# Optimization experiments

Hardware: AMD Instinct MI355X
Metric: run time of the kernel (lower is better)

## Reference

```python
import jax, jax.numpy as jnp
import numpy as np

N = 8000      # num_nodes
U = 64        # num_units
D = 2         # input_dim
K = 2         # max_diffusion_step
E = 64000     # edges per support
B = 32        # batch
F = D + U     # concat feature size = 66
M = 2 * K + 1 # num_matrices = 5


def setup_inputs() -> dict:
    key = jax.random.key(0)
    ks = jax.random.split(key, 10)
    return {
        "inputs": jax.random.normal(ks[0], (B, N * D), dtype=jnp.float32),
        "hx": jax.random.normal(ks[1], (B, N * U), dtype=jnp.float32),
        "row0": jax.random.randint(ks[2], (E,), 0, N, dtype=jnp.int32),
        "col0": jax.random.randint(ks[3], (E,), 0, N, dtype=jnp.int32),
        "val0": jax.random.uniform(ks[4], (E,), dtype=jnp.float32) / 8.0,
        "row1": jax.random.randint(ks[5], (E,), 0, N, dtype=jnp.int32),
        "col1": jax.random.randint(ks[6], (E,), 0, N, dtype=jnp.int32),
        "val1": jax.random.uniform(ks[7], (E,), dtype=jnp.float32) / 8.0,
        "W_ru": jax.random.normal(ks[8], (F * M, 2 * U), dtype=jnp.float32) * 0.05,
        "b_ru": jnp.ones((2 * U,), dtype=jnp.float32),  # bias_start=1.0
        "W_c": jax.random.normal(ks[9], (F * M, U), dtype=jnp.float32) * 0.05,
        "b_c": jnp.zeros((U,), dtype=jnp.float32),       # bias_start=0.0
    }


def _spmm(row, col, val, x):
    # y[r] += val_e * x[c]  for each edge e=(r,c); x: [N, F*B]
    return jax.ops.segment_sum(val[:, None] * x[col], row, num_segments=N)


def _gconv(inputs, state, W, b, supports, output_size):
    # inputs: [B, N*D_in], state: [B, N*D_st]
    x = jnp.concatenate([inputs.reshape(B, N, -1), state.reshape(B, N, -1)], axis=2)  # [B,N,F]
    f = x.shape[2]
    x0 = x.transpose(1, 2, 0).reshape(N, f * B)  # [N, F*B]
    xs = [x0]
    for (row, col, val) in supports:
        x1 = _spmm(row, col, val, x0)
        xs.append(x1)
        xk_1, xk_2 = x1, x0
        for _ in range(2, K + 1):
            x2 = 2.0 * _spmm(row, col, val, xk_1) - xk_2
            xs.append(x2)
            xk_1, xk_2 = x2, xk_1
    m = len(xs)
    # [M,N,F,B] -> [B,N,F,M] -> [B*N, F*M]
    xc = jnp.stack(xs).reshape(m, N, f, B).transpose(3, 1, 2, 0).reshape(B * N, f * m)
    out = xc @ W + b
    return out.reshape(B, N * output_size)


def reference(inputs, hx, row0, col0, val0, row1, col1, val1, W_ru, b_ru, W_c, b_c):
    supports = ((row0, col0, val0), (row1, col1, val1))
    # reset/update gates via graph convolution
    value = jax.nn.sigmoid(_gconv(inputs, hx, W_ru, b_ru, supports, 2 * U))
    value = value.reshape(B, N, 2 * U)
    r = value[..., :U].reshape(B, N * U)
    u = value[..., U:].reshape(B, N * U)
    c = jnp.tanh(_gconv(inputs, r * hx, W_c, b_c, supports, U))
    new_state = u * hx + (1.0 - u) * c
    return new_state
```

## Files before the change

kernel.cpp:

```cpp
#include <hip/hip_runtime.h>
#include <stdint.h>

#define NN 8000
#define UU 64
#define EE 64000
#define BB 32
#define NB 256000
#define HXS 512000
#define SLAB4 256000
#define NT 8

typedef __attribute__((ext_vector_type(8))) __bf16 bf16x8;
typedef __attribute__((ext_vector_type(4))) float f32x4;

__device__ __forceinline__ unsigned short f2bf(float f){
  unsigned int u = __builtin_bit_cast(unsigned int, f);
  u += 0x7fffu + ((u >> 16) & 1u);
  return (unsigned short)(u >> 16);
}
__device__ __forceinline__ unsigned int pack2(float a, float b){
  return (unsigned int)f2bf(a) | ((unsigned int)f2bf(b) << 16);
}
__device__ __forceinline__ float bflo(unsigned int w){ return __builtin_bit_cast(float, w << 16); }
__device__ __forceinline__ float bfhi(unsigned int w){ return __builtin_bit_cast(float, w & 0xffff0000u); }
__device__ __forceinline__ float bfu(unsigned short v){ return __builtin_bit_cast(float, (unsigned int)v << 16); }

__device__ __forceinline__ void acc8(float* a, float v, uint4 q){
  a[0]+=v*bflo(q.x); a[1]+=v*bfhi(q.x); a[2]+=v*bflo(q.y); a[3]+=v*bfhi(q.y);
  a[4]+=v*bflo(q.z); a[5]+=v*bfhi(q.z); a[6]+=v*bflo(q.w); a[7]+=v*bfhi(q.w);
}

__device__ __forceinline__ void stage16(const unsigned short* g, unsigned short* ldsbase){
  __builtin_amdgcn_global_load_lds((const __attribute__((address_space(1))) void*)g,
                                   (__attribute__((address_space(3))) void*)ldsbase, 16, 0, 0);
}

__global__ void k_hist(const int* __restrict__ r0, const int* __restrict__ r1, int* __restrict__ cnt){
  int i = blockIdx.x * 256 + threadIdx.x;
  if (i < 2*EE){
    int s = (i >= EE);
    int r = s ? r1[i - EE] : r0[i];
    atomicAdd(&cnt[s*NN + r], 1);
  }
}

__global__ __launch_bounds__(1024) void k_scan(const int* __restrict__ cnt, int* __restrict__ row_ptr, int* __restrict__ rp_work){
  int sup = blockIdx.x;
  const int* c = cnt + sup*NN;
  __shared__ int part[1024];
  int t = threadIdx.x;
  int loc[8]; int s = 0;
  #pragma unroll
  for (int j=0;j<8;j++){ int idx=t*8+j; int v = (idx<NN)? c[idx]:0; loc[j]=s; s+=v; }
  part[t]=s; __syncthreads();
  for (int o=1;o<1024;o<<=1){
    int v = (t>=o)? part[t-o]:0;
    __syncthreads();
    part[t]+=v;
    __syncthreads();
  }
  int pre = (t>0)? part[t-1]:0;
  #pragma unroll
  for (int j=0;j<8;j++){ int idx=t*8+j; if(idx<NN){ int e=pre+loc[j]; row_ptr[sup*(NN+1)+idx]=e; rp_work[sup*NN+idx]=e; } }
  if (t==1023) row_ptr[sup*(NN+1)+NN] = part[1023];
}

__global__ void k_scatter(const int* __restrict__ r0, const int* __restrict__ c0, const float* __restrict__ v0,
                          const int* __restrict__ r1, const int* __restrict__ c1, const float* __restrict__ v1,
                          int* __restrict__ rp_work, int* __restrict__ col_s, float* __restrict__ val_s){
  int i = blockIdx.x * 256 + threadIdx.x;
  if (i < 2*EE){
    int s = (i >= EE);
    int e = s ? i - EE : i;
    int r  = s ? r1[e] : r0[e];
    int cc = s ? c1[e] : c0[e];
    float vv = s ? v1[e] : v0[e];
    int pos = atomicAdd(&rp_work[s*NN + r], 1);
    col_s[s*EE + pos] = cc;
    val_s[s*EE + pos] = vv;
  }
}

__global__ void k_wpack(const float* __restrict__ W_ru, const float* __restrict__ W_c,
                        unsigned short* __restrict__ Wru_t, unsigned short* __restrict__ Wc_t){
  int i = blockIdx.x * 256 + threadIdx.x;
  int k = i / 192; int oo = i % 192;
  const float* W; int ld, NC; unsigned short* dst; int c;
  if (oo < 128){ W = W_ru; ld = 128; NC = 128; dst = Wru_t; c = oo; }
  else         { W = W_c;  ld = 64;  NC = 64;  dst = Wc_t;  c = oo - 128; }
  int o = 4*(c & 15) + ((c >> 4) & 3);
  int wcol = (c >= 64) ? 64 + o : o;
  float v = 0.f;
  if (k < 330){
    int m, fb;
    if (k < 320){ m = k >> 6; fb = (2 + (k & 63)) * 5; }
    else        { int j = k - 320; m = j >> 1; fb = (j & 1) * 5; }
    if      (m==0) v = W[(fb+0)*ld+wcol] - W[(fb+2)*ld+wcol] - W[(fb+4)*ld+wcol];
    else if (m==1) v = W[(fb+1)*ld+wcol];
    else if (m==2) v = 2.f*W[(fb+2)*ld+wcol];
    else if (m==3) v = W[(fb+3)*ld+wcol];
    else           v = 2.f*W[(fb+4)*ld+wcol];
  }
  int dstoff;
  if (k < 320) dstoff = (k>>6)*NC*64 + c*64 + (k&63);
  else         dstoff = 320*NC + c*32 + (k-320);
  dst[dstoff] = f2bf(v);
}

__global__ void k_x0(const float* __restrict__ inputs, const float* __restrict__ hx,
                     uint4* __restrict__ xs0q, unsigned int* __restrict__ xi0){
  int n = blockIdx.x, t = threadIdx.x;
  int b = t >> 3, ug = t & 7;
  const float4 h0 = *(const float4*)(hx + (size_t)b*HXS + n*64 + ug*8);
  const float4 h1 = *(const float4*)(hx + (size_t)b*HXS + n*64 + ug*8 + 4);
  uint4 o;
  o.x = pack2(h0.x, h0.y); o.y = pack2(h0.z, h0.w);
  o.z = pack2(h1.x, h1.y); o.w = pack2(h1.z, h1.w);
  xs0q[(((size_t)(b>>2)*NN + n)*4 + (b&3))*8 + ug] = o;
  if (t < 32){
    int bb = t;
    const float2 g = *(const float2*)(inputs + (size_t)bb*(NN*2) + n*2);
    xi0[(((size_t)(bb>>2)*NN) + n)*4 + (bb&3)] = pack2(g.x, g.y);
  }
}

template<bool WITH_IN>
__global__ void k_spmm(const int* __restrict__ row_ptr, const int* __restrict__ col_s, const float* __restrict__ val_s,
                       uint4* xs4, uint4* xi4,
                       int srcA, int dstA, int srcB, int dstB){
  int bid = blockIdx.x;
  if (WITH_IN && bid >= 16000){
    int b2 = bid - 16000;
    int s = b2 & 7, supi = (b2 >> 3) & 1, chunk = b2 >> 4;
    int n = chunk*256 + threadIdx.x;
    if (n >= NN) return;
    int msrc = supi ? srcB : srcA, mdst = supi ? dstB : dstA;
    size_t sb = (size_t)(msrc*8 + s)*NN, db = (size_t)(mdst*8 + s)*NN;
    int beg = row_ptr[supi*(NN+1)+n], end = row_ptr[supi*(NN+1)+n+1];
    const int* cs = col_s + supi*EE; const float* vs = val_s + supi*EE;
    float ai[8] = {0.f,0.f,0.f,0.f,0.f,0.f,0.f,0.f};
    for (int e = beg; e < end; ++e){
      int c = cs[e]; float v = vs[e];
      uint4 qi = xi4[sb + c];
      acc8(ai, v, qi);
    }
    uint4 oi;
    oi.x = pack2(ai[0],ai[1]); oi.y = pack2(ai[2],ai[3]); oi.z = pack2(ai[4],ai[5]); oi.w = pack2(ai[6],ai[7]);
    xi4[db + n] = oi;
    return;
  }
  int s  = bid & 7;
  int r2 = bid >> 3;
  int supi = (r2 >= 1000) ? 1 : 0;
  int g = r2 - supi*1000;
  int sub = threadIdx.x >> 5, lane = threadIdx.x & 31;
  int n = g*8 + sub;
  int msrc = supi ? srcB : srcA, mdst = supi ? dstB : dstA;
  size_t sS = (size_t)(msrc*8 + s)*SLAB4;
  size_t dS = (size_t)(mdst*8 + s)*SLAB4;
  int beg = row_ptr[supi*(NN+1)+n], end = row_ptr[supi*(NN+1)+n+1];
  const int* cs = col_s + supi*EE;
  const float* vs = val_s + supi*EE;

  float a[8] = {0.f,0.f,0.f,0.f,0.f,0.f,0.f,0.f};
  int e = beg;
  for (; e + 4 <= end; e += 4){
    int c0=cs[e], c1=cs[e+1], c2=cs[e+2], c3=cs[e+3];
    float v0=vs[e], v1=vs[e+1], v2=vs[e+2], v3=vs[e+3];
    uint4 q0 = xs4[sS + (size_t)c0*32 + lane];
    uint4 q1 = xs4[sS + (size_t)c1*32 + lane];
    uint4 q2 = xs4[sS + (size_t)c2*32 + lane];
    uint4 q3 = xs4[sS + (size_t)c3*32 + lane];
    acc8(a, v0, q0); acc8(a, v1, q1); acc8(a, v2, q2); acc8(a, v3, q3);
  }
  for (; e < end; ++e){
    int c = cs[e]; float v = vs[e];
    uint4 q = xs4[sS + (size_t)c*32 + lane];
    acc8(a, v, q);
  }
  uint4 o;
  o.x = pack2(a[0],a[1]); o.y = pack2(a[2],a[3]); o.z = pack2(a[4],a[5]); o.w = pack2(a[6],a[7]);
  xs4[dS + (size_t)n*32 + lane] = o;
}

template<int NCOL, bool IS_RU>
__global__ __launch_bounds__(256) void k_gemm(unsigned short* xsS,
                                              const unsigned int* __restrict__ xsI,
                                              const unsigned short* __restrict__ Wp,
                                              const float* __restrict__ bias,
                                              const float* __restrict__ hx,
                                              float* cout,
                                              unsigned short* ubuf){
  constexpr int CF = NCOL / 16;
  constexpr int BCH = NCOL*44;
  constexpr int BPT = BCH/256;
  constexpr int MCH = 5*NCOL*8;
  __shared__ unsigned short ring[4][128*64];
  __shared__ unsigned short Bs[5*NCOL*64 + NCOL*32];

  const int t = threadIdx.x;
  const int wv = t >> 6;
  const int l = t & 63;
  const int lr = l & 15;
  const int lg = l >> 4;
  const int tile0 = blockIdx.x * NT;

  #pragma unroll
  for (int i=0;i<BPT;i++){
    int g = t + i*256;
    const unsigned short* gp;
    if (g < MCH){
      int rr = g >> 3, c = g & 7;
      gp = Wp + (size_t)rr*64 + ((c ^ (rr&7)) << 3);
    } else {
      int gt = g - MCH; int rr = gt >> 2, c = gt & 3;
      gp = Wp + (size_t)320*NCOL + rr*32 + ((c ^ (rr&3)) << 3);
    }
    stage16(gp, &Bs[(size_t)(i*256 + wv*64)*8]);
  }

  auto stageA = [&](int rt, int mm, int slot){
    int R0 = (tile0 + rt) << 7;
    #pragma unroll
    for (int i=0;i<4;i++){
      int base = wv*256 + i*64;
      int sl = base + l;
      int rr = sl >> 3, c = sl & 7;
      int row = R0 + rr; int n = row >> 5, b = row & 31;
      const unsigned short* gp = xsS + (size_t)mm*(8*NN*256)
          + ((((size_t)(b>>2))*NN + n)*4 + (b&3))*64 + ((c ^ (rr&7)) << 3);
      stage16(gp, &ring[slot][(size_t)base*8]);
    }
  };

  stageA(0, 0, 0); stageA(0, 1, 1); stageA(0, 2, 2);

  f32x4 acc[2][CF];
  const f32x4 zero = {0.f,0.f,0.f,0.f};
  #pragma unroll
  for (int rf=0; rf<2; rf++)
    #pragma unroll
    for (int cf=0; cf<CF; cf++) acc[rf][cf] = zero;

  unsigned int q[2][5];
  size_t ib[2];

  #pragma unroll 1
  for (int r_=0; r_<NT; ++r_){
    int R0 = (tile0 + r_) << 7;
    #pragma unroll
    for (int m=0; m<5; ++m){
      if (m == 0){
        #pragma unroll
        for (int rf=0; rf<2; rf++){
          int row = R0 + wv*32 + rf*16 + lr;
          int n = row >> 5, b = row & 31;
          ib[rf] = (((size_t)(b>>2))*NN + n)*4 + (b&3);
          #pragma unroll
          for (int mi=0; mi<5; mi++)
            q[rf][mi] = xsI[(size_t)mi*(8*NN*4) + ib[rf]];
        }
      }
      if (r_ == NT-1 && m == 3)      { asm volatile("s_waitcnt vmcnt(4)" ::: "memory"); }
      else if (r_ == NT-1 && m == 4) { asm volatile("s_waitcnt vmcnt(0)" ::: "memory"); }
      else                           { asm volatile("s_waitcnt vmcnt(8)" ::: "memory"); }
      __builtin_amdgcn_s_barrier();
      __builtin_amdgcn_sched_barrier(0);
      if (!(r_ == NT-1 && m >= 2)){
        int mm = (m+3 >= 5) ? m-2 : m+3;
        int rt = (m+3 >= 5) ? r_+1 : r_;
        stageA(rt, mm, (r_*5 + m + 3) & 3);
      }
      const unsigned short* Alc = ring[(r_*5 + m) & 3];
      const unsigned short* Bm  = Bs + m*NCOL*64;
      #pragma unroll
      for (int ks=0; ks<2; ks++){
        bf16x8 af[2];
        #pragma unroll
        for (int rf=0; rf<2; rf++){
          int rr = wv*32 + rf*16 + lr;
          int chunk = (ks*4 + lg) ^ (rr & 7);
          af[rf] = __builtin_bit_cast(bf16x8, *(const uint4*)(Alc + rr*64 + chunk*8));
        }
        #pragma unroll
        for (int cf=0; cf<CF; cf++){
          int col = cf*16 + lr;
          int chunk = (ks*4 + lg) ^ (col & 7);
          bf16x8 bv = __builtin_bit_cast(bf16x8, *(const uint4*)(Bm + col*64 + chunk*8));
          acc[0][cf] = __builtin_amdgcn_mfma_f32_16x16x32_bf16(af[0], bv, acc[0][cf], 0, 0, 0);
          acc[1][cf] = __builtin_amdgcn_mfma_f32_16x16x32_bf16(af[1], bv, acc[1][cf], 0, 0, 0);
        }
      }
    }
    {
      const unsigned short* Bt = Bs + 5*NCOL*64;
      bf16x8 af[2];
      #pragma unroll
      for (int rf=0; rf<2; rf++){
        uint4 qq;
        qq.x = (lg==0) ? q[rf][0] : ((lg==1) ? q[rf][4] : 0u);
        qq.y = (lg==0) ? q[rf][1] : 0u;
        qq.z = (lg==0) ? q[rf][2] : 0u;
        qq.w = (lg==0) ? q[rf][3] : 0u;
        af[rf] = __builtin_bit_cast(bf16x8, qq);
      }
      #pragma unroll
      for (int cf=0; cf<CF; cf++){
        int col = cf*16 + lr;
        int chunk = lg ^ (col & 3);
        bf16x8 bv = __builtin_bit_cast(bf16x8, *(const uint4*)(Bt + col*32 + chunk*8));
        acc[0][cf] = __builtin_amdgcn_mfma_f32_16x16x32_bf16(af[0], bv, acc[0][cf], 0, 0, 0);
        acc[1][cf] = __builtin_amdgcn_mfma_f32_16x16x32_bf16(af[1], bv, acc[1][cf], 0, 0, 0);
      }
    }
    #pragma unroll
    for (int rf=0; rf<2; rf++){
      #pragma unroll
      for (int reg=0; reg<4; reg++){
        int row = R0 + wv*32 + rf*16 + (lg << 2) + reg;
        int n = row >> 5, b = row & 31;
        size_t rowoff = (size_t)b*HXS + (size_t)n*UU;
        size_t slot0 = ((((size_t)(b>>2))*NN + n)*4 + (b&3))*64;
        int o0 = lr << 2;
        if constexpr (IS_RU){
          uint2 hv = *(const uint2*)(xsS + slot0 + o0);
          unsigned short rr4[4], uu4[4];
          #pragma unroll
          for (int cf=0; cf<4; cf++){
            int o = o0 + cf;
            float vr = acc[rf][cf][reg]   + bias[o];
            float vu = acc[rf][cf+4][reg] + bias[64+o];
            float sgr = 1.f/(1.f + __expf(-vr));
            float sgu = 1.f/(1.f + __expf(-vu));
            float h = bfu(((const unsigned short*)&hv)[cf]);
            rr4[cf] = f2bf(sgr * h);
            uu4[cf] = f2bf(sgu);
          }
          *(uint2*)(xsS + slot0 + o0) = *(uint2*)rr4;
          *(uint2*)(ubuf + rowoff + o0) = *(uint2*)uu4;
        } else {
          float4 hv = *(const float4*)(hx + rowoff + o0);
          uint2 uv = *(const uint2*)(ubuf + rowoff + o0);
          float4 ov;
          #pragma unroll
          for (int cf=0; cf<4; cf++){
            float cc = tanhf(acc[rf][cf][reg] + bias[o0+cf]);
            float uu = bfu(((const unsigned short*)&uv)[cf]);
            float h  = ((const float*)&hv)[cf];
            ((float*)&ov)[cf] = uu*h + (1.f - uu)*cc;
          }
          *(float4*)(cout + rowoff + o0) = ov;
        }
      }
    }
    #pragma unroll
    for (int rf=0; rf<2; rf++)
      #pragma unroll
      for (int cf=0; cf<CF; cf++) acc[rf][cf] = zero;
  }
}

extern "C" void kernel_launch(void* const* d_in, const int* in_sizes, int n_in,
                              void* d_out, int out_size, void* d_ws, size_t ws_size,
                              hipStream_t stream){
  const float* inputs = (const float*)d_in[0];
  const float* hx     = (const float*)d_in[1];
  const int*   row0   = (const int*)d_in[2];
  const int*   col0   = (const int*)d_in[3];
  const float* val0   = (const float*)d_in[4];
  const int*   row1   = (const int*)d_in[5];
  const int*   col1   = (const int*)d_in[6];
  const float* val1   = (const float*)d_in[7];
  const float* W_ru   = (const float*)d_in[8];
  const float* b_ru   = (const float*)d_in[9];
  const float* W_c    = (const float*)d_in[10];
  const float* b_c    = (const float*)d_in[11];
  float* out = (float*)d_out;

  char* ws = (char*)d_ws;
  size_t off = 0;
  auto alloc = [&](size_t bytes) -> void* {
    void* p = ws + off;
    off += (bytes + 255) & ~(size_t)255;
    return p;
  };
  unsigned short* xsS   = (unsigned short*)alloc((size_t)5*8*NN*256*2);
  unsigned int*   xsI   = (unsigned int*)  alloc((size_t)5*8*NN*16);
  unsigned short* u_buf = (unsigned short*)alloc((size_t)NB*64*2);
  unsigned short* Wru_t = (unsigned short*)alloc((size_t)128*352*2);
  unsigned short* Wc_t  = (unsigned short*)alloc((size_t)64*352*2);
  int*   row_ptr = (int*)  alloc(2*(NN+1)*4);
  int*   col_s   = (int*)  alloc(2*EE*4);
  float* val_s   = (float*)alloc(2*EE*4);
  int*   cnt     = (int*)  alloc(2*NN*4);
  int*   rp_work = (int*)  alloc(2*NN*4);
  (void)ws_size; (void)in_sizes; (void)n_in; (void)out_size;

  hipMemsetAsync(cnt, 0, 2*NN*4, stream);
  k_hist<<<(2*EE + 255)/256, 256, 0, stream>>>(row0, row1, cnt);
  k_scan<<<2, 1024, 0, stream>>>(cnt, row_ptr, rp_work);
  k_scatter<<<(2*EE + 255)/256, 256, 0, stream>>>(row0, col0, val0, row1, col1, val1, rp_work, col_s, val_s);
  k_wpack<<<(352*192)/256, 256, 0, stream>>>(W_ru, W_c, Wru_t, Wc_t);
  k_x0<<<NN, 256, 0, stream>>>(inputs, hx, (uint4*)xsS, (unsigned int*)xsI);

  uint4* xs4 = (uint4*)xsS;
  uint4* xi4 = (uint4*)xsI;

  k_spmm<true ><<<16512, 256, 0, stream>>>(row_ptr, col_s, val_s, xs4, xi4, 0, 1, 0, 3);
  k_spmm<true ><<<16512, 256, 0, stream>>>(row_ptr, col_s, val_s, xs4, xi4, 1, 2, 3, 4);
  k_gemm<128, true><<<250, 256, 0, stream>>>(xsS, xsI, Wru_t, b_ru, hx, nullptr, u_buf);

  k_spmm<false><<<16000, 256, 0, stream>>>(row_ptr, col_s, val_s, xs4, xi4, 0, 1, 0, 3);
  k_spmm<false><<<16000, 256, 0, stream>>>(row_ptr, col_s, val_s, xs4, xi4, 1, 2, 3, 4);
  k_gemm<64, false><<<250, 256, 0, stream>>>(xsS, xsI, Wc_t, b_c, hx, out, u_buf);
}
```

Before: 428.6 us.

## Re-slab state layout by batch pairs and restructure GEMM to per-tile direct loads

Changes the bf16 state layout from 8 slabs of 4 batches to 16 slabs of 2 batches, so each SpMM row gather is 256 bytes handled by 16 lanes, with slabs spread across XCDs. The GEMM drops its multi-tile LDS ring for A and instead loads A fragments straight from global memory into registers. Only the weights are double-buffered in LDS, one tile per block, with 2000 blocks and an occupancy hint. The last SpMM pass of each gconv uses nontemporal stores. This aims to improve cache locality per XCD and GEMM parallelism, at the cost of less A reuse in LDS and more barriers.

Result: faster. 393.9 us (-8.1%).

```diff
diff --git a/kernel.cpp b/kernel.cpp
--- a/kernel.cpp
+++ b/kernel.cpp
@@ -7,11 +7,10 @@
 #define BB 32
 #define NB 256000
 #define HXS 512000
-#define SLAB4 256000
-#define NT 8
 
 typedef __attribute__((ext_vector_type(8))) __bf16 bf16x8;
 typedef __attribute__((ext_vector_type(4))) float f32x4;
+typedef __attribute__((ext_vector_type(4))) unsigned int u32x4;
 
 __device__ __forceinline__ unsigned short f2bf(float f){
   unsigned int u = __builtin_bit_cast(unsigned int, f);
@@ -116,7 +115,7 @@
   uint4 o;
   o.x = pack2(h0.x, h0.y); o.y = pack2(h0.z, h0.w);
   o.z = pack2(h1.x, h1.y); o.w = pack2(h1.z, h1.w);
-  xs0q[(((size_t)(b>>2)*NN + n)*4 + (b&3))*8 + ug] = o;
+  xs0q[(size_t)(b>>1)*(NN*16) + (size_t)n*16 + (b&1)*8 + ug] = o;
   if (t < 32){
     int bb = t;
     const float2 g = *(const float2*)(inputs + (size_t)bb*(NN*2) + n*2);
@@ -124,7 +123,7 @@
   }
 }
 
-template<bool WITH_IN>
+template<bool WITH_IN, bool NTDST>
 __global__ void k_spmm(const int* __restrict__ row_ptr, const int* __restrict__ col_s, const float* __restrict__ val_s,
                        uint4* xs4, uint4* xi4,
                        int srcA, int dstA, int srcB, int dstB){
@@ -146,18 +145,23 @@
     }
     uint4 oi;
     oi.x = pack2(ai[0],ai[1]); oi.y = pack2(ai[2],ai[3]); oi.z = pack2(ai[4],ai[5]); oi.w = pack2(ai[6],ai[7]);
-    xi4[db + n] = oi;
+    if (NTDST){
+      u32x4 ov = {oi.x, oi.y, oi.z, oi.w};
+      __builtin_nontemporal_store(ov, (u32x4*)&xi4[db + n]);
+    } else xi4[db + n] = oi;
     return;
   }
-  int s  = bid & 7;
-  int r2 = bid >> 3;
-  int supi = (r2 >= 1000) ? 1 : 0;
-  int g = r2 - supi*1000;
-  int sub = threadIdx.x >> 5, lane = threadIdx.x & 31;
-  int n = g*8 + sub;
+  int xcd = bid & 7;
+  int seq = bid >> 3;
+  int supi = (seq >= 1000) ? 1 : 0;
+  int seq2 = seq - supi*1000;
+  int slice = (seq2 < 500) ? xcd : (xcd + 8);
+  int group = (seq2 < 500) ? seq2 : (seq2 - 500);
+  int sub = threadIdx.x >> 4, lane = threadIdx.x & 15;
+  int n = group*16 + sub;
   int msrc = supi ? srcB : srcA, mdst = supi ? dstB : dstA;
-  size_t sS = (size_t)(msrc*8 + s)*SLAB4;
-  size_t dS = (size_t)(mdst*8 + s)*SLAB4;
+  size_t sS = (size_t)msrc*(NN*256) + (size_t)slice*(NN*16);
+  size_t dS = (size_t)mdst*(NN*256) + (size_t)slice*(NN*16);
   int beg = row_ptr[supi*(NN+1)+n], end = row_ptr[supi*(NN+1)+n+1];
   const int* cs = col_s + supi*EE;
   const float* vs = val_s + supi*EE;
@@ -167,73 +171,99 @@
   for (; e + 4 <= end; e += 4){
     int c0=cs[e], c1=cs[e+1], c2=cs[e+2], c3=cs[e+3];
     float v0=vs[e], v1=vs[e+1], v2=vs[e+2], v3=vs[e+3];
-    uint4 q0 = xs4[sS + (size_t)c0*32 + lane];
-    uint4 q1 = xs4[sS + (size_t)c1*32 + lane];
-    uint4 q2 = xs4[sS + (size_t)c2*32 + lane];
-    uint4 q3 = xs4[sS + (size_t)c3*32 + lane];
+    uint4 q0 = xs4[sS + (size_t)c0*16 + lane];
+    uint4 q1 = xs4[sS + (size_t)c1*16 + lane];
+    uint4 q2 = xs4[sS + (size_t)c2*16 + lane];
+    uint4 q3 = xs4[sS + (size_t)c3*16 + lane];
     acc8(a, v0, q0); acc8(a, v1, q1); acc8(a, v2, q2); acc8(a, v3, q3);
   }
   for (; e < end; ++e){
     int c = cs[e]; float v = vs[e];
-    uint4 q = xs4[sS + (size_t)c*32 + lane];
+    uint4 q = xs4[sS + (size_t)c*16 + lane];
     acc8(a, v, q);
   }
   uint4 o;
   o.x = pack2(a[0],a[1]); o.y = pack2(a[2],a[3]); o.z = pack2(a[4],a[5]); o.w = pack2(a[6],a[7]);
-  xs4[dS + (size_t)n*32 + lane] = o;
+  if (NTDST){
+    u32x4 ov = {o.x, o.y, o.z, o.w};
+    __builtin_nontemporal_store(ov, (u32x4*)&xs4[dS + (size_t)n*16 + lane]);
+  } else xs4[dS + (size_t)n*16 + lane] = o;
 }
 
 template<int NCOL, bool IS_RU>
-__global__ __launch_bounds__(256) void k_gemm(unsigned short* xsS,
-                                              const unsigned int* __restrict__ xsI,
-                                              const unsigned short* __restrict__ Wp,
-                                              const float* __restrict__ bias,
-                                              const float* __restrict__ hx,
-                                              float* cout,
-                                              unsigned short* ubuf){
+__global__ __launch_bounds__(256, 3) void k_gemm(unsigned short* xsS,
+                                                 const unsigned int* __restrict__ xsI,
+                                                 const unsigned short* __restrict__ Wp,
+                                                 const float* __restrict__ bias,
+                                                 const float* __restrict__ hx,
+                                                 float* cout,
+                                                 unsigned short* ubuf){
   constexpr int CF = NCOL / 16;
-  constexpr int BCH = NCOL*44;
-  constexpr int BPT = BCH/256;
-  constexpr int MCH = 5*NCOL*8;
-  __shared__ unsigned short ring[4][128*64];
-  __shared__ unsigned short Bs[5*NCOL*64 + NCOL*32];
-
+  __shared__ unsigned short Bl[2][NCOL*64];
+  __shared__ unsigned short Bt[NCOL*32];
   const int t = threadIdx.x;
   const int wv = t >> 6;
   const int l = t & 63;
   const int lr = l & 15;
   const int lg = l >> 4;
-  const int tile0 = blockIdx.x * NT;
-
-  #pragma unroll
-  for (int i=0;i<BPT;i++){
-    int g = t + i*256;
-    const unsigned short* gp;
-    if (g < MCH){
+  const int R0 = blockIdx.x * 128;
+
+  auto stageB = [&](int m, int buf){
+    #pragma unroll
+    for (int i=0;i<NCOL*8/256;i++){
+      int g = t + i*256;
       int rr = g >> 3, c = g & 7;
-      gp = Wp + (size_t)rr*64 + ((c ^ (rr&7)) << 3);
-    } else {
-      int gt = g - MCH; int rr = gt >> 2, c = gt & 3;
-      gp = Wp + (size_t)320*NCOL + rr*32 + ((c ^ (rr&3)) << 3);
-    }
-    stage16(gp, &Bs[(size_t)(i*256 + wv*64)*8]);
-  }
-
-  auto stageA = [&](int rt, int mm, int slot){
-    int R0 = (tile0 + rt) << 7;
-    #pragma unroll
-    for (int i=0;i<4;i++){
-      int base = wv*256 + i*64;
-      int sl = base + l;
-      int rr = sl >> 3, c = sl & 7;
-      int row = R0 + rr; int n = row >> 5, b = row & 31;
-      const unsigned short* gp = xsS + (size_t)mm*(8*NN*256)
-          + ((((size_t)(b>>2))*NN + n)*4 + (b&3))*64 + ((c ^ (rr&7)) << 3);
-      stage16(gp, &ring[slot][(size_t)base*8]);
+      const unsigned short* gp = Wp + (size_t)(m*NCOL + rr)*64 + ((c ^ (rr&7)) << 3);
+      stage16(gp, &Bl[buf][(size_t)(i*256 + wv*64)*8]);
     }
   };
 
-  stageA(0, 0, 0); stageA(0, 1, 1); stageA(0, 2, 2);
+  size_t abase[2];
+  #pragma unroll
+  for (int rf=0; rf<2; rf++){
+    int row = R0 + wv*32 + rf*16 + lr;
+    int n = row >> 5, b = row & 31;
+    abase[rf] = (size_t)(b>>1)*(NN*128) + (size_t)n*128 + (b&1)*64;
+  }
+  auto loadA = [&](int m, uint4* dst){
+    #pragma unroll
+    for (int ks=0; ks<2; ks++)
+      #pragma unroll
+      for (int rf=0; rf<2; rf++)
+        dst[ks*2+rf] = *(const uint4*)(xsS + (size_t)m*(NN*2048) + abase[rf] + ks*32 + lg*8);
+  };
+
+  uint4 aC[4], aN[4];
+  loadA(0, aC);
+  uint4 aT[2];
+  #pragma unroll
+  for (int rf=0; rf<2; rf++){
+    int row = R0 + wv*32 + rf*16 + lr;
+    int n = row >> 5, b = row & 31;
+    size_t ib = (((size_t)(b>>2))*NN + n)*4 + (b&3);
+    unsigned int q0=0u,q1=0u,q2=0u,q3=0u;
+    if (lg == 0){
+      q0 = xsI[ib];
+      q1 = xsI[(size_t)8*NN*4 + ib];
+      q2 = xsI[(size_t)16*NN*4 + ib];
+      q3 = xsI[(size_t)24*NN*4 + ib];
+    } else if (lg == 1){
+      q0 = xsI[(size_t)32*NN*4 + ib];
+    }
+    uint4 qq; qq.x=q0; qq.y=q1; qq.z=q2; qq.w=q3;
+    aT[rf] = qq;
+  }
+  stageB(0, 0);
+  {
+    #pragma unroll
+    for (int i=0;i<NCOL*4/256;i++){
+      int g = t + i*256;
+      int rr = g >> 2, c = g & 3;
+      const unsigned short* gp = Wp + (size_t)320*NCOL + rr*32 + ((c ^ (rr&3)) << 3);
+      stage16(gp, &Bt[(size_t)(i*256 + wv*64)*8]);
+    }
+  }
+  __syncthreads();
 
   f32x4 acc[2][CF];
   const f32x4 zero = {0.f,0.f,0.f,0.f};
@@ -242,121 +272,77 @@
     #pragma unroll
     for (int cf=0; cf<CF; cf++) acc[rf][cf] = zero;
 
-  unsigned int q[2][5];
-  size_t ib[2];
-
-  #pragma unroll 1
-  for (int r_=0; r_<NT; ++r_){
-    int R0 = (tile0 + r_) << 7;
-    #pragma unroll
-    for (int m=0; m<5; ++m){
-      if (m == 0){
-        #pragma unroll
-        for (int rf=0; rf<2; rf++){
-          int row = R0 + wv*32 + rf*16 + lr;
-          int n = row >> 5, b = row & 31;
-          ib[rf] = (((size_t)(b>>2))*NN + n)*4 + (b&3);
-          #pragma unroll
-          for (int mi=0; mi<5; mi++)
-            q[rf][mi] = xsI[(size_t)mi*(8*NN*4) + ib[rf]];
-        }
-      }
-      if (r_ == NT-1 && m == 3)      { asm volatile("s_waitcnt vmcnt(4)" ::: "memory"); }
-      else if (r_ == NT-1 && m == 4) { asm volatile("s_waitcnt vmcnt(0)" ::: "memory"); }
-      else                           { asm volatile("s_waitcnt vmcnt(8)" ::: "memory"); }
-      __builtin_amdgcn_s_barrier();
-      __builtin_amdgcn_sched_barrier(0);
-      if (!(r_ == NT-1 && m >= 2)){
-        int mm = (m+3 >= 5) ? m-2 : m+3;
-        int rt = (m+3 >= 5) ? r_+1 : r_;
-        stageA(rt, mm, (r_*5 + m + 3) & 3);
-      }
-      const unsigned short* Alc = ring[(r_*5 + m) & 3];
-      const unsigned short* Bm  = Bs + m*NCOL*64;
-      #pragma unroll
-      for (int ks=0; ks<2; ks++){
-        bf16x8 af[2];
-        #pragma unroll
-        for (int rf=0; rf<2; rf++){
-          int rr = wv*32 + rf*16 + lr;
-          int chunk = (ks*4 + lg) ^ (rr & 7);
-          af[rf] = __builtin_bit_cast(bf16x8, *(const uint4*)(Alc + rr*64 + chunk*8));
-        }
-        #pragma unroll
-        for (int cf=0; cf<CF; cf++){
-          int col = cf*16 + lr;
-          int chunk = (ks*4 + lg) ^ (col & 7);
-          bf16x8 bv = __builtin_bit_cast(bf16x8, *(const uint4*)(Bm + col*64 + chunk*8));
-          acc[0][cf] = __builtin_amdgcn_mfma_f32_16x16x32_bf16(af[0], bv, acc[0][cf], 0, 0, 0);
-          acc[1][cf] = __builtin_amdgcn_mfma_f32_16x16x32_bf16(af[1], bv, acc[1][cf], 0, 0, 0);
-        }
-      }
-    }
-    {
-      const unsigned short* Bt = Bs + 5*NCOL*64;
-      bf16x8 af[2];
-      #pragma unroll
-      for (int rf=0; rf<2; rf++){
-        uint4 qq;
-        qq.x = (lg==0) ? q[rf][0] : ((lg==1) ? q[rf][4] : 0u);
-        qq.y = (lg==0) ? q[rf][1] : 0u;
-        qq.z = (lg==0) ? q[rf][2] : 0u;
-        qq.w = (lg==0) ? q[rf][3] : 0u;
-        af[rf] = __builtin_bit_cast(bf16x8, qq);
-      }
+  #pragma unroll
+  for (int m=0; m<5; m++){
+    int cur = m & 1;
+    if (m < 4){
+      stageB(m+1, cur^1);
+      loadA(m+1, aN);
+    }
+    #pragma unroll
+    for (int ks=0; ks<2; ks++){
       #pragma unroll
       for (int cf=0; cf<CF; cf++){
         int col = cf*16 + lr;
-        int chunk = lg ^ (col & 3);
-        bf16x8 bv = __builtin_bit_cast(bf16x8, *(const uint4*)(Bt + col*32 + chunk*8));
-        acc[0][cf] = __builtin_amdgcn_mfma_f32_16x16x32_bf16(af[0], bv, acc[0][cf], 0, 0, 0);
-        acc[1][cf] = __builtin_amdgcn_mfma_f32_16x16x32_bf16(af[1], bv, acc[1][cf], 0, 0, 0);
+        int chunk = (ks*4 + lg) ^ (col & 7);
+        bf16x8 bv = __builtin_bit_cast(bf16x8, *(const uint4*)(&Bl[cur][col*64 + chunk*8]));
+        acc[0][cf] = __builtin_amdgcn_mfma_f32_16x16x32_bf16(__builtin_bit_cast(bf16x8, aC[ks*2+0]), bv, acc[0][cf], 0, 0, 0);
+        acc[1][cf] = __builtin_amdgcn_mfma_f32_16x16x32_bf16(__builtin_bit_cast(bf16x8, aC[ks*2+1]), bv, acc[1][cf], 0, 0, 0);
       }
     }
-    #pragma unroll
-    for (int rf=0; rf<2; rf++){
-      #pragma unroll
-      for (int reg=0; reg<4; reg++){
-        int row = R0 + wv*32 + rf*16 + (lg << 2) + reg;
-        int n = row >> 5, b = row & 31;
-        size_t rowoff = (size_t)b*HXS + (size_t)n*UU;
-        size_t slot0 = ((((size_t)(b>>2))*NN + n)*4 + (b&3))*64;
-        int o0 = lr << 2;
-        if constexpr (IS_RU){
-          uint2 hv = *(const uint2*)(xsS + slot0 + o0);
-          unsigned short rr4[4], uu4[4];
-          #pragma unroll
-          for (int cf=0; cf<4; cf++){
-            int o = o0 + cf;
-            float vr = acc[rf][cf][reg]   + bias[o];
-            float vu = acc[rf][cf+4][reg] + bias[64+o];
-            float sgr = 1.f/(1.f + __expf(-vr));
-            float sgu = 1.f/(1.f + __expf(-vu));
-            float h = bfu(((const unsigned short*)&hv)[cf]);
-            rr4[cf] = f2bf(sgr * h);
-            uu4[cf] = f2bf(sgu);
-          }
-          *(uint2*)(xsS + slot0 + o0) = *(uint2*)rr4;
-          *(uint2*)(ubuf + rowoff + o0) = *(uint2*)uu4;
-        } else {
-          float4 hv = *(const float4*)(hx + rowoff + o0);
-          uint2 uv = *(const uint2*)(ubuf + rowoff + o0);
-          float4 ov;
-          #pragma unroll
-          for (int cf=0; cf<4; cf++){
-            float cc = tanhf(acc[rf][cf][reg] + bias[o0+cf]);
-            float uu = bfu(((const unsigned short*)&uv)[cf]);
-            float h  = ((const float*)&hv)[cf];
-            ((float*)&ov)[cf] = uu*h + (1.f - uu)*cc;
-          }
-          *(float4*)(cout + rowoff + o0) = ov;
+    __syncthreads();
+    #pragma unroll
+    for (int i=0;i<4;i++) aC[i] = aN[i];
+  }
+
+  #pragma unroll
+  for (int cf=0; cf<CF; cf++){
+    int col = cf*16 + lr;
+    int chunk = lg ^ (col & 3);
+    bf16x8 bv = __builtin_bit_cast(bf16x8, *(const uint4*)(&Bt[col*32 + chunk*8]));
+    acc[0][cf] = __builtin_amdgcn_mfma_f32_16x16x32_bf16(__builtin_bit_cast(bf16x8, aT[0]), bv, acc[0][cf], 0, 0, 0);
+    acc[1][cf] = __builtin_amdgcn_mfma_f32_16x16x32_bf16(__builtin_bit_cast(bf16x8, aT[1]), bv, acc[1][cf], 0, 0, 0);
+  }
+
+  #pragma unroll
+  for (int rf=0; rf<2; rf++){
+    #pragma unroll
+    for (int reg=0; reg<4; reg++){
+      int row = R0 + wv*32 + rf*16 + (lg << 2) + reg;
+      int n = row >> 5, b = row & 31;
+      size_t rowoff = (size_t)b*HXS + (size_t)n*UU;
+      size_t slot0 = (size_t)(b>>1)*(NN*128) + (size_t)n*128 + (b&1)*64;
+      int o0 = lr << 2;
+      if constexpr (IS_RU){
+        uint2 hv = *(const uint2*)(xsS + slot0 + o0);
+        unsigned short rr4[4], uu4[4];
+        #pragma unroll
+        for (int cf=0; cf<4; cf++){
+          int o = o0 + cf;
+          float vr = acc[rf][cf][reg]   + bias[o];
+          float vu = acc[rf][cf+4][reg] + bias[64+o];
+          float sgr = 1.f/(1.f + __expf(-vr));
+          float sgu = 1.f/(1.f + __expf(-vu));
+          float h = bfu(((const unsigned short*)&hv)[cf]);
+          rr4[cf] = f2bf(sgr * h);
+          uu4[cf] = f2bf(sgu);
         }
+        *(uint2*)(xsS + slot0 + o0) = *(uint2*)rr4;
+        *(uint2*)(ubuf + rowoff + o0) = *(uint2*)uu4;
+      } else {
+        float4 hv = *(const float4*)(hx + rowoff + o0);
+        uint2 uv = *(const uint2*)(ubuf + rowoff + o0);
+        float4 ov;
+        #pragma unroll
+        for (int cf=0; cf<4; cf++){
+          float cc = tanhf(acc[rf][cf][reg] + bias[o0+cf]);
+          float uu = bfu(((const unsigned short*)&uv)[cf]);
+          float h  = ((const float*)&hv)[cf];
+          ((float*)&ov)[cf] = uu*h + (1.f - uu)*cc;
+        }
+        *(float4*)(cout + rowoff + o0) = ov;
       }
     }
-    #pragma unroll
-    for (int rf=0; rf<2; rf++)
-      #pragma unroll
-      for (int cf=0; cf<CF; cf++) acc[rf][cf] = zero;
   }
 }
 
@@ -384,7 +370,7 @@
     off += (bytes + 255) & ~(size_t)255;
     return p;
   };
-  unsigned short* xsS   = (unsigned short*)alloc((size_t)5*8*NN*256*2);
+  unsigned short* xsS   = (unsigned short*)alloc((size_t)5*NN*2048*2);
   unsigned int*   xsI   = (unsigned int*)  alloc((size_t)5*8*NN*16);
   unsigned short* u_buf = (unsigned short*)alloc((size_t)NB*64*2);
   unsigned short* Wru_t = (unsigned short*)alloc((size_t)128*352*2);
@@ -406,11 +392,11 @@
   uint4* xs4 = (uint4*)xsS;
   uint4* xi4 = (uint4*)xsI;
 
-  k_spmm<true ><<<16512, 256, 0, stream>>>(row_ptr, col_s, val_s, xs4, xi4, 0, 1, 0, 3);
-  k_spmm<true ><<<16512, 256, 0, stream>>>(row_ptr, col_s, val_s, xs4, xi4, 1, 2, 3, 4);
-  k_gemm<128, true><<<250, 256, 0, stream>>>(xsS, xsI, Wru_t, b_ru, hx, nullptr, u_buf);
-
-  k_spmm<false><<<16000, 256, 0, stream>>>(row_ptr, col_s, val_s, xs4, xi4, 0, 1, 0, 3);
-  k_spmm<false><<<16000, 256, 0, stream>>>(row_ptr, col_s, val_s, xs4, xi4, 1, 2, 3, 4);
-  k_gemm<64, false><<<250, 256, 0, stream>>>(xsS, xsI, Wc_t, b_c, hx, out, u_buf);
-}
+  k_spmm<true , false><<<16512, 256, 0, stream>>>(row_ptr, col_s, val_s, xs4, xi4, 0, 1, 0, 3);
+  k_spmm<true , true ><<<16512, 256, 0, stream>>>(row_ptr, col_s, val_s, xs4, xi4, 1, 2, 3, 4);
+  k_gemm<128, true><<<2000, 256, 0, stream>>>(xsS, xsI, Wru_t, b_ru, hx, nullptr, u_buf);
+
+  k_spmm<false, false><<<16000, 256, 0, stream>>>(row_ptr, col_s, val_s, xs4, xi4, 0, 1, 0, 3);
+  k_spmm<false, true ><<<16000, 256, 0, stream>>>(row_ptr, col_s, val_s, xs4, xi4, 1, 2, 3, 4);
+  k_gemm<64, false><<<2000, 256, 0, stream>>>(xsS, xsI, Wc_t, b_c, hx, out, u_buf);
+}
```
